# Optimization experiments

Measured on AMD Instinct MI355X. Metric: run time of the kernel, lower is better.

## Reference

```python
import jax, jax.numpy as jnp
import numpy as np

C = 300      # caption feature dim (word2vec)
OQK = 75     # in_dim // k = 300 // 4 -> query/key channels
H = 128      # adapt_img_hidden (base_proj dim)
LAT = 1024   # image latent size
EPS = 1e-5   # BatchNorm eps


def setup_inputs() -> dict:
    key = jax.random.key(0)
    ks = jax.random.split(key, 16)
    r = lambda i, shape, s=0.05: jax.random.normal(ks[i], shape, dtype=jnp.float32) * s
    return dict(
        img_embed=jax.random.normal(ks[0], (128, 36, LAT), dtype=jnp.float32),
        cap_embed=jax.random.normal(ks[1], (64, 32, C), dtype=jnp.float32),
        # adapt_img: Linear(1024, 128)
        adapt_W=r(2, (H, LAT)), adapt_b=jnp.zeros((H,), jnp.float32),
        # query ProjConv1d: kernel Linear(H, OQK*C), bias Linear(H, OQK), BatchNorm1d(OQK)
        qk_W=r(3, (OQK * C, H)), qk_b=r(4, (OQK * C,)),
        qb_W=r(5, (OQK, H)), qb_b=jnp.zeros((OQK,), jnp.float32),
        q_bn_s=jnp.ones((OQK,), jnp.float32), q_bn_b=jnp.zeros((OQK,), jnp.float32),
        # key ProjConv1d
        kk_W=r(6, (OQK * C, H)), kk_b=r(7, (OQK * C,)),
        kb_W=r(8, (OQK, H)), kb_b=jnp.zeros((OQK,), jnp.float32),
        k_bn_s=jnp.ones((OQK,), jnp.float32), k_bn_b=jnp.zeros((OQK,), jnp.float32),
        # value ProjConv1d: kernel Linear(H, C*C), bias Linear(H, C), BatchNorm1d(C)
        vk_W=r(9, (C * C, H)), vk_b=r(10, (C * C,)),
        vb_W=r(11, (C, H)), vb_b=jnp.zeros((C,), jnp.float32),
        v_bn_s=jnp.ones((C,), jnp.float32), v_bn_b=jnp.zeros((C,), jnp.float32),
        gamma=jnp.float32(0.5),  # residual attention gate (torch inits to 0; 0.5 exercises the path)
        # sim_proj MLP: 300 -> 512 -> 64 -> 1 with BatchNorm+ReLU (dropout = identity at eval)
        W1=r(12, (512, C)), b1=jnp.zeros((512,), jnp.float32),
        bn1_s=jnp.ones((512,), jnp.float32), bn1_b=jnp.zeros((512,), jnp.float32),
        W2=r(13, (64, 512)), b2=jnp.zeros((64,), jnp.float32),
        bn2_s=jnp.ones((64,), jnp.float32), bn2_b=jnp.zeros((64,), jnp.float32),
        W3=r(14, (1, 64)), b3=jnp.zeros((1,), jnp.float32),
    )


def _bn_kernel(kern, s, b):
    # torch: BatchNorm1d(out)(kernel.permute(1,0,2)) with kernel (out, in, ks=1)
    # -> per out-channel stats over the `in` axis (train-mode batch stats)
    mu = kern.mean(axis=1, keepdims=True)
    var = kern.var(axis=1, keepdims=True)
    return (kern - mu) / jnp.sqrt(var + EPS) * s[:, None] + b[:, None]


def _bn_batch(x, s, b):
    # BatchNorm1d over batch axis of (N, C) activations (train-mode stats)
    mu = x.mean(axis=0, keepdims=True)
    var = x.var(axis=0, keepdims=True)
    return (x - mu) / jnp.sqrt(var + EPS) * s + b


def reference(img_embed, cap_embed, adapt_W, adapt_b,
              qk_W, qk_b, qb_W, qb_b, q_bn_s, q_bn_b,
              kk_W, kk_b, kb_W, kb_b, k_bn_s, k_bn_b,
              vk_W, vk_b, vb_W, vb_b, v_bn_s, v_bn_b,
              gamma, W1, b1, bn1_s, bn1_b, W2, b2, bn2_s, bn2_b, W3, b3):
    cap = cap_embed.transpose(0, 2, 1)                      # (Bc, C, T)
    img_mean = img_embed.transpose(0, 2, 1).mean(-1)        # (Bi, LAT): mean over 36 regions
    base = img_mean @ adapt_W.T + adapt_b                   # (Bi, H)

    def per_image(bp):
        # hypernet-generated 1x1 conv kernels, batchnorm-normalized
        Kq = _bn_kernel((qk_W @ bp + qk_b).reshape(OQK, C), q_bn_s, q_bn_b)
        Kk = _bn_kernel((kk_W @ bp + kk_b).reshape(OQK, C), k_bn_s, k_bn_b)
        Kv = _bn_kernel((vk_W @ bp + vk_b).reshape(C, C), v_bn_s, v_bn_b)
        bq = qb_W @ bp + qb_b
        bk = kb_W @ bp + kb_b
        bv = vb_W @ bp + vb_b
        q = jnp.einsum('oc,nct->not', Kq, cap) + bq[:, None]    # (Bc, OQK, T)
        k = jnp.einsum('oc,nct->not', Kk, cap) + bk[:, None]    # (Bc, OQK, T)
        v = jnp.einsum('oc,nct->not', Kv, cap) + bv[:, None]    # (Bc, C, T)
        attn = jax.nn.softmax(jnp.einsum('not,nos->nts', q, k), axis=-1)  # (Bc, T, T)
        sa = jnp.einsum('ncs,nts->nct', v, attn)                # out = V @ attn^T
        x = (gamma * sa + cap).max(-1)                          # (Bc, C): max-pool over tokens
        h = jax.nn.relu(_bn_batch(x @ W1.T + b1, bn1_s, bn1_b))
        h = jax.nn.relu(_bn_batch(h @ W2.T + b2, bn2_s, bn2_b))
        return (h @ W3.T + b3)[:, 0]                            # (Bc,)

    return jax.vmap(per_image)(base)                            # (Bi, Bc)
```

## Files before the change

kernel.cpp:

```cpp
#include <hip/hip_runtime.h>
#include <math.h>

#define EPSB 1e-5f

static const long OFS_BASE  = 0;
static const long OFS_BALL  = 16384;
static const long OFS_CAPB  = 212992;
static const long OFS_RAWP  = 868352;
static const long OFS_X     = 15286272;
static const long OFS_H2    = 17743872;
static const long OFS_BASP  = 18268160;
static const long OFS_H1    = OFS_RAWP;

using bf16x8 = __attribute__((ext_vector_type(8))) __bf16;
using f32x4  = __attribute__((ext_vector_type(4))) float;
#define MFMA16(a, b, c) __builtin_amdgcn_mfma_f32_16x16x32_bf16(a, b, c, 0, 0, 0)

__device__ inline ushort f2bf(float f) {
  const unsigned u = __float_as_uint(f);
  return (ushort)((u + 0x7FFFu + ((u >> 16) & 1u)) >> 16);
}
__device__ inline float bf2f(ushort h) { return __uint_as_float(((unsigned)h) << 16); }

__global__ void __launch_bounds__(256) k_mb(const float* __restrict__ img,
                                            const float* __restrict__ W,
                                            const float* __restrict__ b,
                                            float* __restrict__ base) {
  __shared__ float m_s[1024];
  __shared__ float part[128];
  const int i = blockIdx.x, tid = threadIdx.x;
#pragma unroll
  for (int lc = 0; lc < 4; ++lc) {
    const int l = lc * 256 + tid;
    const float* p = img + (size_t)i * 36864 + l;
    float s = 0.f;
#pragma unroll
    for (int r = 0; r < 36; ++r) s += p[r * 1024];
    m_s[l] = s * (1.0f / 36.0f);
  }
  __syncthreads();
  const int o = tid & 127, hk = tid >> 7;
  const float* wr = W + (size_t)o * 1024 + hk * 512;
  const float* ms = m_s + hk * 512;
  float acc = 0.f;
#pragma unroll 4
  for (int l = 0; l < 512; ++l) acc = fmaf(ms[l], wr[l], acc);
  if (hk) part[o] = acc;
  __syncthreads();
  if (!hk) base[i * 128 + o] = acc + part[o] + b[o];
}

__global__ void __launch_bounds__(256) k_prep(
    const float* __restrict__ qbW, const float* __restrict__ qbb,
    const float* __restrict__ kbW, const float* __restrict__ kbb,
    const float* __restrict__ vbW, const float* __restrict__ vbb,
    const float* __restrict__ base, float* __restrict__ ball,
    const float* __restrict__ cap, ushort* __restrict__ capP,
    ushort* __restrict__ basP) {
  __shared__ float shm[32 * 301];
  const int bid = blockIdx.x, tid = threadIdx.x;
  if (bid < 256) {
    const int i = bid >> 1;
    if (tid < 128) shm[tid] = base[i * 128 + tid];
    __syncthreads();
    const int o = (bid & 1) * 256 + tid;
    const float* Wr = nullptr;
    float bb = 0.0f;
    if (o < 75)                   { Wr = qbW + (size_t)o * 128;         bb = qbb[o]; }
    else if (o >= 96 && o < 171)  { Wr = kbW + (size_t)(o - 96) * 128;  bb = kbb[o - 96]; }
    else if (o >= 192 && o < 492) { Wr = vbW + (size_t)(o - 192) * 128; bb = vbb[o - 192]; }
    float acc = 0.0f;
    if (Wr) {
#pragma unroll 4
      for (int h = 0; h < 128; ++h) acc = fmaf(Wr[h], shm[h], acc);
      acc += bb;
    }
    ball[i * 512 + o] = acc;
  } else if (bid < 320) {
    const int n = bid - 256;
    const float* capn = cap + (size_t)n * 9600;
    {
      const int r = tid >> 3, c8 = tid & 7;
      for (int m = 0; m < 38; ++m) {
        const int c = c8 + 8 * m;
        if (c < 300) shm[r * 301 + c] = capn[r * 300 + c];
      }
    }
    __syncthreads();
    ushort* dst = capP + (size_t)n * 20480;
    for (int u = 0; u < 10; ++u) {
      const int ul = tid + 256 * u;
      const int unit = ul >> 6, lane = ul & 63;
      const int nt = unit / 20, rem = unit % 20;
      const int ks = rem >> 1, pl = rem & 1;
      const int kg = lane >> 4, lr = lane & 15;
      const int t = nt * 16 + lr;
      ushort o8[8];
#pragma unroll
      for (int e = 0; e < 8; ++e) {
        const int c = 32 * ks + 8 * kg + e;
        const float val = (c < 300) ? shm[t * 301 + c] : 0.f;
        const ushort hi = f2bf(val);
        o8[e] = pl ? f2bf(val - bf2f(hi)) : hi;
      }
      uint4 pk;
      pk.x = (uint)o8[0] | ((uint)o8[1] << 16);
      pk.y = (uint)o8[2] | ((uint)o8[3] << 16);
      pk.z = (uint)o8[4] | ((uint)o8[5] << 16);
      pk.w = (uint)o8[6] | ((uint)o8[7] << 16);
      *reinterpret_cast<uint4*>(dst + unit * 512 + lane * 8) = pk;
    }
  } else {
    const int half = bid - 320;
    for (int m = 0; m < 8; ++m) {
      const int u = tid + 256 * m;
      const int ln = u & 63, unit = u >> 6;
      const int it = unit >> 3, ks = (unit >> 1) & 3, pl = unit & 1;
      const int i = half * 64 + it * 16 + (ln & 15);
      const int h = ks * 32 + (ln >> 4) * 8;
      ushort o8[8];
#pragma unroll
      for (int e = 0; e < 8; ++e) {
        const float v = base[(size_t)i * 128 + h + e];
        const ushort hi = f2bf(v);
        o8[e] = pl ? f2bf(v - bf2f(hi)) : hi;
      }
      uint4 pk;
      pk.x = (uint)o8[0] | ((uint)o8[1] << 16);
      pk.y = (uint)o8[2] | ((uint)o8[3] << 16);
      pk.z = (uint)o8[4] | ((uint)o8[5] << 16);
      pk.w = (uint)o8[6] | ((uint)o8[7] << 16);
      *reinterpret_cast<uint4*>(basP + (size_t)(half * 32 + unit) * 512 + ln * 8) = pk;
    }
  }
}

__global__ void __launch_bounds__(256) k_hyp4(
    const float* __restrict__ qkW, const float* __restrict__ qkb,
    const float* __restrict__ kkW, const float* __restrict__ kkb,
    const float* __restrict__ vkW, const float* __restrict__ vkb,
    const float* __restrict__ qs, const float* __restrict__ qb,
    const float* __restrict__ ks_, const float* __restrict__ kb_,
    const float* __restrict__ vs, const float* __restrict__ vb,
    const ushort* __restrict__ basP, ushort* __restrict__ kall) {
  __shared__ float smem[19760];
  __shared__ float scl[64], shf[64];
  const int g = blockIdx.x, half = blockIdx.y, tid = threadIdx.x;
  const int i0g = half * 64;
  const int ot = g >> 4, lr = g & 15;
  const bool isV = (g >= 192);
  if ((g >= 80 && g < 96) || (g >= 176 && g < 192)) return;

  const float* Wb = nullptr;
  const float* bvec = nullptr;
  float bns = 0.f, bnb = 0.f;
  if (g < 75)                    { Wb = qkW + (size_t)g * 38400;          bvec = qkb + g * 300;          bns = qs[g];        bnb = qb[g]; }
  else if (g >= 96 && g < 171)   { Wb = kkW + (size_t)(g - 96) * 38400;   bvec = kkb + (g - 96) * 300;   bns = ks_[g - 96];  bnb = kb_[g - 96]; }
  else if (g >= 192 && g < 492)  { Wb = vkW + (size_t)(g - 192) * 38400;  bvec = vkb + (g - 192) * 300;  bns = vs[g - 192];  bnb = vb[g - 192]; }

  if (!Wb) {
    const uint4 z = make_uint4(0, 0, 0, 0);
    if (!isV) {
      for (int m = 0; m < 20; ++m) {
        const int idx = tid + 256 * m;
        const int ii = idx & 63, zz = idx >> 6;
        const int kg2 = zz & 3, pl = (zz >> 2) & 1, ks2 = zz >> 3;
        const size_t off = (size_t)(i0g + ii) * 225280 +
                           (size_t)(ot * 20 + ks2 * 2 + pl) * 512 + (kg2 * 16 + lr) * 8;
        *reinterpret_cast<uint4*>(kall + off) = z;
      }
    } else {
      for (int m = 0; m < 10; ++m) {
        const int idx = tid + 256 * m;
        const int ii = idx & 63, zz = idx >> 6;
        const int kg2 = zz & 3, ks2 = zz >> 2;
        const size_t off = (size_t)(i0g + ii) * 225280 +
                           (size_t)(240 + (ot - 12) * 10 + ks2) * 512 + (kg2 * 16 + lr) * 8;
        *reinterpret_cast<uint4*>(kall + off) = z;
      }
    }
    return;
  }

  const int lane = tid & 63, w = tid >> 6;
  const int lrow = lane & 15, kg = lane >> 4;
  ushort* Af = reinterpret_cast<ushort*>(smem + 9760);

  f32x4 acc[19];
#pragma unroll
  for (int ct = 0; ct < 19; ++ct) acc[ct] = (f32x4){0.f, 0.f, 0.f, 0.f};

  for (int hc = 0; hc < 4; ++hc) {
    __syncthreads();
    for (int m = 0; m < 10; ++m) {
      const int u = tid + 256 * m;
      if (u < 2432) {
        const int c = u >> 3, h4 = (u & 7) * 4;
        float4 wv = make_float4(0.f, 0.f, 0.f, 0.f);
        if (c < 300) wv = *reinterpret_cast<const float4*>(Wb + (size_t)c * 128 + hc * 32 + h4);
        smem[(h4 + 0) * 305 + c] = wv.x;
        smem[(h4 + 1) * 305 + c] = wv.y;
        smem[(h4 + 2) * 305 + c] = wv.z;
        smem[(h4 + 3) * 305 + c] = wv.w;
      }
    }
    __syncthreads();
    for (int m = 0; m < 5; ++m) {
      const int u = tid + 256 * m;
      if (u < 1216) {
        const int ln = u & 63, ct = u >> 6;
        const int cc = ct * 16 + (ln & 15);
        const int hb = (ln >> 4) * 8;
        ushort h8[8], l8[8];
#pragma unroll
        for (int e = 0; e < 8; ++e) {
          const float v = smem[(hb + e) * 305 + cc];
          const ushort hi = f2bf(v);
          h8[e] = hi;
          l8[e] = f2bf(v - bf2f(hi));
        }
        uint4 ph, pl4;
        ph.x = (uint)h8[0] | ((uint)h8[1] << 16);
        ph.y = (uint)h8[2] | ((uint)h8[3] << 16);
        ph.z = (uint)h8[4] | ((uint)h8[5] << 16);
        ph.w = (uint)h8[6] | ((uint)h8[7] << 16);
        pl4.x = (uint)l8[0] | ((uint)l8[1] << 16);
        pl4.y = (uint)l8[2] | ((uint)l8[3] << 16);
        pl4.z = (uint)l8[4] | ((uint)l8[5] << 16);
        pl4.w = (uint)l8[6] | ((uint)l8[7] << 16);
        *reinterpret_cast<uint4*>(&Af[(ct * 2 + 0) * 512 + ln * 8]) = ph;
        *reinterpret_cast<uint4*>(&Af[(ct * 2 + 1) * 512 + ln * 8]) = pl4;
      }
    }
    const bf16x8 Bh = *reinterpret_cast<const bf16x8*>(
        basP + (size_t)(half * 32 + w * 8 + hc * 2 + 0) * 512 + lane * 8);
    const bf16x8 Bl = *reinterpret_cast<const bf16x8*>(
        basP + (size_t)(half * 32 + w * 8 + hc * 2 + 1) * 512 + lane * 8);
    __syncthreads();
#pragma unroll
    for (int ct = 0; ct < 19; ++ct) {
      const bf16x8 Ah = *reinterpret_cast<const bf16x8*>(&Af[(ct * 2 + 0) * 512 + lane * 8]);
      const bf16x8 Al = *reinterpret_cast<const bf16x8*>(&Af[(ct * 2 + 1) * 512 + lane * 8]);
      acc[ct] = MFMA16(Ah, Bh, acc[ct]);
      acc[ct] = MFMA16(Ah, Bl, acc[ct]);
      acc[ct] = MFMA16(Al, Bh, acc[ct]);
    }
  }
  __syncthreads();
#pragma unroll
  for (int ct = 0; ct < 19; ++ct)
#pragma unroll
    for (int r = 0; r < 4; ++r) {
      const int c = ct * 16 + kg * 4 + r;
      if (c < 300) smem[c * 65 + w * 16 + lrow] = acc[ct][r] + bvec[c];
    }
  __syncthreads();
  {
    const int si = tid >> 2, p = tid & 3;
    float s1 = 0.f, s2 = 0.f;
    for (int c = p; c < 300; c += 4) {
      const float x = smem[c * 65 + si];
      s1 += x;
      s2 += x * x;
    }
    s1 += __shfl_xor(s1, 1); s2 += __shfl_xor(s2, 1);
    s1 += __shfl_xor(s1, 2); s2 += __shfl_xor(s2, 2);
    const float mu = s1 * (1.0f / 300.0f);
    const float var = s2 * (1.0f / 300.0f) - mu * mu;
    const float scale = bns / sqrtf(var + EPSB);
    if (p == 0) { scl[si] = scale; shf[si] = bnb - mu * scale; }
  }
  __syncthreads();
  if (!isV) {
    for (int m = 0; m < 20; ++m) {
      const int idx = tid + 256 * m;
      const int ii = idx & 63, zz = idx >> 6;
      const int kg2 = zz & 3, pl = (zz >> 2) & 1, ks2 = zz >> 3;
      const float sc = scl[ii], sh = shf[ii];
      ushort o8[8];
#pragma unroll
      for (int e = 0; e < 8; ++e) {
        const int c = ks2 * 32 + kg2 * 8 + e;
        float val = 0.f;
        if (c < 300) val = fmaf(smem[c * 65 + ii], sc, sh);
        const ushort hi = f2bf(val);
        o8[e] = pl ? f2bf(val - bf2f(hi)) : hi;
      }
      uint4 pk;
      pk.x = (uint)o8[0] | ((uint)o8[1] << 16);
      pk.y = (uint)o8[2] | ((uint)o8[3] << 16);
      pk.z = (uint)o8[4] | ((uint)o8[5] << 16);
      pk.w = (uint)o8[6] | ((uint)o8[7] << 16);
      const size_t off = (size_t)(i0g + ii) * 225280 +
                         (size_t)(ot * 20 + ks2 * 2 + pl) * 512 + (kg2 * 16 + lr) * 8;
      *reinterpret_cast<uint4*>(kall + off) = pk;
    }
  } else {
    for (int m = 0; m < 10; ++m) {
      const int idx = tid + 256 * m;
      const int ii = idx & 63, zz = idx >> 6;
      const int kg2 = zz & 3, ks2 = zz >> 2;
      const float sc = scl[ii], sh = shf[ii];
      ushort o8[8];
#pragma unroll
      for (int e = 0; e < 8; ++e) {
        const int c = ks2 * 32 + kg2 * 8 + e;
        float val = 0.f;
        if (c < 300) val = fmaf(smem[c * 65 + ii], sc, sh);
        o8[e] = f2bf(val);
      }
      uint4 pk;
      pk.x = (uint)o8[0] | ((uint)o8[1] << 16);
      pk.y = (uint)o8[2] | ((uint)o8[3] << 16);
      pk.z = (uint)o8[4] | ((uint)o8[5] << 16);
      pk.w = (uint)o8[6] | ((uint)o8[7] << 16);
      const size_t off = (size_t)(i0g + ii) * 225280 +
                         (size_t)(240 + (ot - 12) * 10 + ks2) * 512 + (kg2 * 16 + lr) * 8;
      *reinterpret_cast<uint4*>(kall + off) = pk;
    }
  }
}

__global__ void __launch_bounds__(256, 4) k_attn12(
    const float* __restrict__ cap, const ushort* __restrict__ kall,
    const ushort* __restrict__ capP, const float* __restrict__ ball,
    const float* __restrict__ gptr, float* __restrict__ x_all) {
  __shared__ ushort qkp[24 * 512];
  __shared__ float sc_s[32 * 36];
  __shared__ ushort at_p[2 * 2 * 64 * 8];
  const int bid = blockIdx.x;
  const int xcd = bid & 7, q = bid >> 3;
  const int i = xcd * 16 + (q >> 6), n = q & 63;
  const int tid = threadIdx.x;
  const int lane = tid & 63, w = tid >> 6;
  const int lrow = lane & 15, kg = lane >> 4;
  const float gamma = gptr[0];
  const ushort* kpL = kall + (size_t)i * 225280 + lane * 8;
  const ushort* cpL = capP + (size_t)n * 20480 + lane * 8;
  const float* bal = ball + i * 512;
  const bool oddw = (w & 1);

  {
    f32x4 acc[3][2];
#pragma unroll
    for (int a = 0; a < 3; ++a)
#pragma unroll
      for (int b2 = 0; b2 < 2; ++b2) acc[a][b2] = (f32x4){0.f, 0.f, 0.f, 0.f};
    bf16x8 AhA[3], AlA[3], AhB[3], AlB[3];
#pragma unroll
    for (int mt = 0; mt < 3; ++mt)
      if (!oddw || mt < 2) {
        const ushort* p = kpL + (size_t)((w * 3 + mt) * 20) * 512;
        AhA[mt] = *reinterpret_cast<const bf16x8*>(p);
        AlA[mt] = *reinterpret_cast<const bf16x8*>(p + 512);
      }
#pragma unroll
    for (int kp = 0; kp < 5; ++kp) {
      {
        const int ks = 2 * kp;
        bf16x8 Bh[2], Bl[2];
#pragma unroll
        for (int nt = 0; nt < 2; ++nt) {
          const ushort* p = cpL + (size_t)(nt * 20 + ks * 2) * 512;
          Bh[nt] = *reinterpret_cast<const bf16x8*>(p);
          Bl[nt] = *reinterpret_cast<const bf16x8*>(p + 512);
        }
#pragma unroll
        for (int mt = 0; mt < 3; ++mt)
          if (!oddw || mt < 2) {
            const ushort* p = kpL + (size_t)((w * 3 + mt) * 20 + (ks + 1) * 2) * 512;
            AhB[mt] = *reinterpret_cast<const bf16x8*>(p);
            AlB[mt] = *reinterpret_cast<const bf16x8*>(p + 512);
          }
#pragma unroll
        for (int mt = 0; mt < 3; ++mt)
          if (!oddw || mt < 2)
#pragma unroll
            for (int nt = 0; nt < 2; ++nt) {
              acc[mt][nt] = MFMA16(AhA[mt], Bh[nt], acc[mt][nt]);
              acc[mt][nt] = MFMA16(AhA[mt], Bl[nt], acc[mt][nt]);
              acc[mt][nt] = MFMA16(AlA[mt], Bh[nt], acc[mt][nt]);
            }
      }
      {
        const int ks = 2 * kp + 1;
        bf16x8 Bh[2], Bl[2];
#pragma unroll
        for (int nt = 0; nt < 2; ++nt) {
          const ushort* p = cpL + (size_t)(nt * 20 + ks * 2) * 512;
          Bh[nt] = *reinterpret_cast<const bf16x8*>(p);
          Bl[nt] = *reinterpret_cast<const bf16x8*>(p + 512);
        }
        if (kp < 4) {
#pragma unroll
          for (int mt = 0; mt < 3; ++mt)
            if (!oddw || mt < 2) {
              const ushort* p = kpL + (size_t)((w * 3 + mt) * 20 + (ks + 1) * 2) * 512;
              AhA[mt] = *reinterpret_cast<const bf16x8*>(p);
              AlA[mt] = *reinterpret_cast<const bf16x8*>(p + 512);
            }
        }
#pragma unroll
        for (int mt = 0; mt < 3; ++mt)
          if (!oddw || mt < 2)
#pragma unroll
            for (int nt = 0; nt < 2; ++nt) {
              acc[mt][nt] = MFMA16(AhB[mt], Bh[nt], acc[mt][nt]);
              acc[mt][nt] = MFMA16(AhB[mt], Bl[nt], acc[mt][nt]);
              acc[mt][nt] = MFMA16(AlB[mt], Bh[nt], acc[mt][nt]);
            }
      }
    }
#pragma unroll
    for (int mt = 0; mt < 3; ++mt)
#pragma unroll
      for (int nt = 0; nt < 2; ++nt) {
        const int og0 = w * 48 + mt * 16 + kg * 4;
        const int os0 = (w < 2) ? og0 : og0 - 96;
        const int ub = ((w < 2) ? 0 : 12) + nt * 6 + (os0 >> 5) * 2;
        const int lp = ((os0 & 31) >> 3) * 16 + lrow;
        const int e0 = os0 & 7;
        ushort h4[4], l4[4];
#pragma unroll
        for (int r = 0; r < 4; ++r) {
          const float val = acc[mt][nt][r] + bal[og0 + r];
          const ushort hi = f2bf(val);
          h4[r] = hi;
          l4[r] = f2bf(val - bf2f(hi));
        }
        uint2 ph, pl2;
        ph.x = (uint)h4[0] | ((uint)h4[1] << 16);
        ph.y = (uint)h4[2] | ((uint)h4[3] << 16);
        pl2.x = (uint)l4[0] | ((uint)l4[1] << 16);
        pl2.y = (uint)l4[2] | ((uint)l4[3] << 16);
        *reinterpret_cast<uint2*>(&qkp[(ub + 0) * 512 + lp * 8 + e0]) = ph;
        *reinterpret_cast<uint2*>(&qkp[(ub + 1) * 512 + lp * 8 + e0]) = pl2;
      }
  }
  __syncthreads();

  {
    const int tt = w >> 1, st = w & 1;
    bf16x8 Aq[3][2], Bk[3][2];
#pragma unroll
    for (int k3 = 0; k3 < 3; ++k3)
#pragma unroll
      for (int pl = 0; pl < 2; ++pl) {
        Aq[k3][pl] = *reinterpret_cast<const bf16x8*>(&qkp[(tt * 6 + k3 * 2 + pl) * 512 + lane * 8]);
        Bk[k3][pl] = *reinterpret_cast<const bf16x8*>(&qkp[(12 + st * 6 + k3 * 2 + pl) * 512 + lane * 8]);
      }
    f32x4 D = (f32x4){0.f, 0.f, 0.f, 0.f};
#pragma unroll
    for (int k3 = 0; k3 < 3; ++k3) {
      D = MFMA16(Aq[k3][0], Bk[k3][0], D);
      D = MFMA16(Aq[k3][0], Bk[k3][1], D);
      D = MFMA16(Aq[k3][1], Bk[k3][0], D);
      D = MFMA16(Aq[k3][1], Bk[k3][1], D);
    }
#pragma unroll
    for (int r = 0; r < 4; ++r)
      sc_s[(tt * 16 + kg * 4 + r) * 36 + st * 16 + lrow] = D[r];
  }
  __syncthreads();

  {
    const int sg = tid & 7, tq = tid >> 3;
    const int s0 = sg * 4;
    const float4 sv = *reinterpret_cast<const float4*>(&sc_s[tq * 36 + s0]);
    float sc[4] = {sv.x, sv.y, sv.z, sv.w};
    float m = fmaxf(fmaxf(sc[0], sc[1]), fmaxf(sc[2], sc[3]));
    m = fmaxf(m, __shfl_xor(m, 1));
    m = fmaxf(m, __shfl_xor(m, 2));
    m = fmaxf(m, __shfl_xor(m, 4));
    float ev[4], ssum = 0.f;
#pragma unroll
    for (int u = 0; u < 4; ++u) { ev[u] = expf(sc[u] - m); ssum += ev[u]; }
    ssum += __shfl_xor(ssum, 1);
    ssum += __shfl_xor(ssum, 2);
    ssum += __shfl_xor(ssum, 4);
    const float inv = 1.0f / ssum;
    const int tt = tq >> 4, lrp = tq & 15, kgp = sg >> 1, eb = (sg & 1) * 4;
    ushort h4[4], l4[4];
#pragma unroll
    for (int u = 0; u < 4; ++u) {
      const float val = ev[u] * inv;
      const ushort hi = f2bf(val);
      h4[u] = hi;
      l4[u] = f2bf(val - bf2f(hi));
    }
    uint2 ph, pl2;
    ph.x = (uint)h4[0] | ((uint)h4[1] << 16);
    ph.y = (uint)h4[2] | ((uint)h4[3] << 16);
    pl2.x = (uint)l4[0] | ((uint)l4[1] << 16);
    pl2.y = (uint)l4[2] | ((uint)l4[3] << 16);
    *reinterpret_cast<uint2*>(&at_p[((tt * 2 + 0) * 64 + kgp * 16 + lrp) * 8 + eb]) = ph;
    *reinterpret_cast<uint2*>(&at_p[((tt * 2 + 1) * 64 + kgp * 16 + lrp) * 8 + eb]) = pl2;
  }
  __syncthreads();

  ushort* vt = qkp;
#pragma unroll
  for (int ch = 0; ch < 2; ++ch) {
    const int TB = 12 + ch * 12;
    const int RB = TB * 16;
    const int nmt = ch ? 2 : 3;
    f32x4 vacc[3][2];
#pragma unroll
    for (int a = 0; a < 3; ++a)
#pragma unroll
      for (int b2 = 0; b2 < 2; ++b2) vacc[a][b2] = (f32x4){0.f, 0.f, 0.f, 0.f};
    bf16x8 AvA[3], AvB[3];
    for (int mi = 0; mi < nmt; ++mi)
      AvA[mi] = *reinterpret_cast<const bf16x8*>(
          kpL + (size_t)(240 + (TB - 12 + w + mi * 4) * 10) * 512);
#pragma unroll
    for (int kp = 0; kp < 5; ++kp) {
      {
        const int ks = 2 * kp;
        bf16x8 Ch[2];
#pragma unroll
        for (int nt = 0; nt < 2; ++nt)
          Ch[nt] = *reinterpret_cast<const bf16x8*>(cpL + (size_t)(nt * 20 + ks * 2) * 512);
        for (int mi = 0; mi < nmt; ++mi)
          AvB[mi] = *reinterpret_cast<const bf16x8*>(
              kpL + (size_t)(240 + (TB - 12 + w + mi * 4) * 10 + ks + 1) * 512);
        for (int mi = 0; mi < nmt; ++mi)
#pragma unroll
          for (int nt = 0; nt < 2; ++nt)
            vacc[mi][nt] = MFMA16(Ch[nt], AvA[mi], vacc[mi][nt]);
      }
      {
        const int ks = 2 * kp + 1;
        bf16x8 Ch[2];
#pragma unroll
        for (int nt = 0; nt < 2; ++nt)
          Ch[nt] = *reinterpret_cast<const bf16x8*>(cpL + (size_t)(nt * 20 + ks * 2) * 512);
        if (kp < 4) {
          for (int mi = 0; mi < nmt; ++mi)
            AvA[mi] = *reinterpret_cast<const bf16x8*>(
                kpL + (size_t)(240 + (TB - 12 + w + mi * 4) * 10 + ks + 1) * 512);
        }
        for (int mi = 0; mi < nmt; ++mi)
#pragma unroll
          for (int nt = 0; nt < 2; ++nt)
            vacc[mi][nt] = MFMA16(Ch[nt], AvB[mi], vacc[mi][nt]);
      }
    }
    if (ch) __syncthreads();
    for (int mi = 0; mi < nmt; ++mi) {
      const int tile = w + mi * 4;
      const float bb = bal[RB + tile * 16 + lrow];
#pragma unroll
      for (int nt = 0; nt < 2; ++nt) {
        const int lpv = (nt * 2 + (kg >> 1)) * 16 + lrow;
        const int e0v = (kg & 1) * 4;
        ushort h4[4], l4[4];
#pragma unroll
        for (int r = 0; r < 4; ++r) {
          const float val = vacc[mi][nt][r] + bb;
          const ushort hi = f2bf(val);
          h4[r] = hi;
          l4[r] = f2bf(val - bf2f(hi));
        }
        uint2 ph, pl2;
        ph.x = (uint)h4[0] | ((uint)h4[1] << 16);
        ph.y = (uint)h4[2] | ((uint)h4[3] << 16);
        pl2.x = (uint)l4[0] | ((uint)l4[1] << 16);
        pl2.y = (uint)l4[2] | ((uint)l4[3] << 16);
        *reinterpret_cast<uint2*>(&vt[((tile * 2 + 0) * 64 + lpv) * 8 + e0v]) = ph;
        *reinterpret_cast<uint2*>(&vt[((tile * 2 + 1) * 64 + lpv) * 8 + e0v]) = pl2;
      }
    }
    __syncthreads();
    {
      bf16x8 ah[2], al[2];
#pragma unroll
      for (int tt = 0; tt < 2; ++tt) {
        ah[tt] = *reinterpret_cast<const bf16x8*>(&at_p[((tt * 2 + 0) * 64 + lane) * 8]);
        al[tt] = *reinterpret_cast<const bf16x8*>(&at_p[((tt * 2 + 1) * 64 + lane) * 8]);
      }
      const int npw = ch ? 2 : 3;
      for (int j = 0; j < npw; ++j) {
        const int ct = w * npw + j;
        const int c0 = ch * 192 + ct * 16 + (lane >> 4) * 4;
        const bf16x8 vh  = *reinterpret_cast<const bf16x8*>(&vt[((ct * 2 + 0) * 64 + lane) * 8]);
        const bf16x8 vl8 = *reinterpret_cast<const bf16x8*>(&vt[((ct * 2 + 1) * 64 + lane) * 8]);
        f32x4 a0 = (f32x4){0.f, 0.f, 0.f, 0.f}, a1 = (f32x4){0.f, 0.f, 0.f, 0.f};
        a0 = MFMA16(vh, ah[0], a0);
        a0 = MFMA16(vh, al[0], a0);
        a0 = MFMA16(vl8, ah[0], a0);
        a1 = MFMA16(vh, ah[1], a1);
        a1 = MFMA16(vh, al[1], a1);
        a1 = MFMA16(vl8, ah[1], a1);
        if (c0 < 300) {
          const int t0 = lane & 15;
          const float4 c4a = *reinterpret_cast<const float4*>(&cap[(size_t)n * 9600 + t0 * 300 + c0]);
          const float4 c4b = *reinterpret_cast<const float4*>(&cap[(size_t)n * 9600 + (t0 + 16) * 300 + c0]);
          float mx[4];
          mx[0] = fmaxf(fmaf(gamma, a0[0], c4a.x), fmaf(gamma, a1[0], c4b.x));
          mx[1] = fmaxf(fmaf(gamma, a0[1], c4a.y), fmaf(gamma, a1[1], c4b.y));
          mx[2] = fmaxf(fmaf(gamma, a0[2], c4a.z), fmaf(gamma, a1[2], c4b.z));
          mx[3] = fmaxf(fmaf(gamma, a0[3], c4a.w), fmaf(gamma, a1[3], c4b.w));
#pragma unroll
          for (int mmask = 1; mmask < 16; mmask <<= 1)
#pragma unroll
            for (int r = 0; r < 4; ++r) mx[r] = fmaxf(mx[r], __shfl_xor(mx[r], mmask));
          if ((lane & 15) == 0)
            *reinterpret_cast<float4*>(&x_all[((size_t)i * 64 + n) * 300 + c0]) =
                make_float4(mx[0], mx[1], mx[2], mx[3]);
        }
      }
    }
  }
}

__global__ void __launch_bounds__(256, 4) k_h1b(
    const float* __restrict__ x_all, const float* __restrict__ W1,
    const float* __restrict__ b1, const float* __restrict__ bn1s,
    const float* __restrict__ bn1b, float* __restrict__ h1) {
  __shared__ float xt[32 * 68];
  __shared__ float wt[32 * 132];
  __shared__ float sc1[128], sh1[128];
  const int ec = blockIdx.x, i = blockIdx.y, tid = threadIdx.x;
  const int e0c = ec * 128;
  const int eg = tid & 15, ng = tid >> 4;
  const int e0 = eg * 8, n0 = ng * 4;
  float acc[4][8] = {};
  for (int cb = 0; cb < 10; ++cb) {
    const int c0 = cb * 32;
    __syncthreads();
    for (int k = 0; k < 8; ++k) {
      const int idx = tid + 256 * k;
      const int nn = idx >> 5, cl = idx & 31;
      const int c = c0 + cl;
      xt[cl * 68 + nn] = (c < 300) ? x_all[((size_t)i * 64 + nn) * 300 + c] : 0.0f;
    }
    for (int k = 0; k < 16; ++k) {
      const int idx = tid + 256 * k;
      const int ee = idx >> 5, cl = idx & 31;
      const int c = c0 + cl;
      wt[cl * 132 + ee] = (c < 300) ? W1[(size_t)(e0c + ee) * 300 + c] : 0.0f;
    }
    __syncthreads();
#pragma unroll 4
    for (int cl = 0; cl < 32; ++cl) {
      const float4 xv = *reinterpret_cast<const float4*>(&xt[cl * 68 + n0]);
      const float4 wa = *reinterpret_cast<const float4*>(&wt[cl * 132 + e0]);
      const float4 wb = *reinterpret_cast<const float4*>(&wt[cl * 132 + e0 + 4]);
      const float xv4[4] = {xv.x, xv.y, xv.z, xv.w};
      const float wv8[8] = {wa.x, wa.y, wa.z, wa.w, wb.x, wb.y, wb.z, wb.w};
#pragma unroll
      for (int u = 0; u < 4; ++u)
#pragma unroll
        for (int v = 0; v < 8; ++v) acc[u][v] = fmaf(xv4[u], wv8[v], acc[u][v]);
    }
  }
  float b1v[8];
#pragma unroll
  for (int v = 0; v < 8; ++v) b1v[v] = b1[e0c + e0 + v];
  float val[4][8];
#pragma unroll
  for (int u = 0; u < 4; ++u)
#pragma unroll
    for (int v = 0; v < 8; ++v) val[u][v] = acc[u][v] + b1v[v];
  __syncthreads();
  float* ps1 = xt;
  float* ps2 = wt;
#pragma unroll
  for (int v = 0; v < 8; ++v) {
    float su = 0.f, sq = 0.f;
#pragma unroll
    for (int u = 0; u < 4; ++u) { su += val[u][v]; sq += val[u][v] * val[u][v]; }
    ps1[ng * 132 + e0 + v] = su;
    ps2[ng * 132 + e0 + v] = sq;
  }
  __syncthreads();
  if (tid < 128) {
    const int e = tid;
    float s1 = 0.f, s2 = 0.f;
#pragma unroll 4
    for (int gq = 0; gq < 16; ++gq) { s1 += ps1[gq * 132 + e]; s2 += ps2[gq * 132 + e]; }
    const float mu = s1 * (1.0f / 64.0f);
    const float var = s2 * (1.0f / 64.0f) - mu * mu;
    const float scale = bn1s[e0c + e] / sqrtf(var + EPSB);
    sc1[e] = scale;
    sh1[e] = bn1b[e0c + e] - mu * scale;
  }
  __syncthreads();
#pragma unroll
  for (int u = 0; u < 4; ++u) {
    float o8[8];
#pragma unroll
    for (int v = 0; v < 8; ++v)
      o8[v] = fmaxf(fmaf(val[u][v], sc1[e0 + v], sh1[e0 + v]), 0.0f);
    float* dst = h1 + ((size_t)i * 64 + n0 + u) * 512 + e0c + e0;
    *reinterpret_cast<float4*>(dst) = make_float4(o8[0], o8[1], o8[2], o8[3]);
    *reinterpret_cast<float4*>(dst + 4) = make_float4(o8[4], o8[5], o8[6], o8[7]);
  }
}

__global__ void __launch_bounds__(256) k_h2(
    const float* __restrict__ h1, const float* __restrict__ W2,
    const float* __restrict__ b2, float* __restrict__ h2buf) {
  __shared__ float h1s[32 * 517];
  const int jn = blockIdx.x, i = blockIdx.y, tid = threadIdx.x;
  const int bn = jn * 32;
  for (int m = 0; m < 64; ++m) {
    const int idx = tid + 256 * m;
    h1s[(idx >> 9) * 517 + (idx & 511)] = h1[((size_t)i * 64 + bn) * 512 + idx];
  }
  __syncthreads();
  const int dg = tid & 15, ng2 = tid >> 4;
  const int d0 = dg * 4, n0 = ng2 * 2;
  float a0[4] = {}, a1[4] = {};
#pragma unroll 4
  for (int e = 0; e < 512; ++e) {
    const float h0 = h1s[n0 * 517 + e];
    const float h1v = h1s[(n0 + 1) * 517 + e];
#pragma unroll
    for (int v = 0; v < 4; ++v) {
      const float wv = W2[(size_t)(d0 + v) * 512 + e];
      a0[v] = fmaf(h0, wv, a0[v]);
      a1[v] = fmaf(h1v, wv, a1[v]);
    }
  }
  const float4 bb = *reinterpret_cast<const float4*>(&b2[d0]);
  float* dst0 = h2buf + ((size_t)i * 64 + bn + n0) * 64 + d0;
  *reinterpret_cast<float4*>(dst0) = make_float4(a0[0] + bb.x, a0[1] + bb.y, a0[2] + bb.z, a0[3] + bb.w);
  *reinterpret_cast<float4*>(dst0 + 64) = make_float4(a1[0] + bb.x, a1[1] + bb.y, a1[2] + bb.z, a1[3] + bb.w);
}

__global__ void __launch_bounds__(256) k_out(
    const float* __restrict__ h2buf, const float* __restrict__ bn2s,
    const float* __restrict__ bn2b, const float* __restrict__ W3,
    const float* __restrict__ b3, float* __restrict__ out) {
  __shared__ float h2s[64 * 65];
  const int i = blockIdx.x, tid = threadIdx.x;
  for (int m = 0; m < 16; ++m) {
    const int idx = tid + 256 * m;
    h2s[(idx >> 6) * 65 + (idx & 63)] = h2buf[(size_t)i * 4096 + idx];
  }
  __syncthreads();
  if (tid < 64) {
    const int d = tid;
    float s1 = 0.f, s2 = 0.f;
    for (int nn = 0; nn < 64; ++nn) {
      const float v = h2s[nn * 65 + d];
      s1 += v;
      s2 += v * v;
    }
    const float mu = s1 * (1.0f / 64.0f);
    const float var = s2 * (1.0f / 64.0f) - mu * mu;
    const float scale = bn2s[d] / sqrtf(var + EPSB);
    const float shift = bn2b[d] - mu * scale;
    for (int nn = 0; nn < 64; ++nn)
      h2s[nn * 65 + d] = fmaxf(fmaf(h2s[nn * 65 + d], scale, shift), 0.0f);
  }
  __syncthreads();
  if (tid < 64) {
    const int nn = tid;
    float acc = b3[0];
    for (int d = 0; d < 64; ++d) acc = fmaf(h2s[nn * 65 + d], W3[d], acc);
    out[i * 64 + nn] = acc;
  }
}

extern "C" void kernel_launch(void* const* d_in, const int* in_sizes, int n_in,
                              void* d_out, int out_size, void* d_ws, size_t ws_size,
                              hipStream_t stream) {
  const float* img  = (const float*)d_in[0];
  const float* cap  = (const float*)d_in[1];
  const float* adW  = (const float*)d_in[2];
  const float* adb  = (const float*)d_in[3];
  const float* qkW  = (const float*)d_in[4];
  const float* qkb  = (const float*)d_in[5];
  const float* qbW  = (const float*)d_in[6];
  const float* qbb  = (const float*)d_in[7];
  const float* qbns = (const float*)d_in[8];
  const float* qbnb = (const float*)d_in[9];
  const float* kkW  = (const float*)d_in[10];
  const float* kkb  = (const float*)d_in[11];
  const float* kbW  = (const float*)d_in[12];
  const float* kbb  = (const float*)d_in[13];
  const float* kbns = (const float*)d_in[14];
  const float* kbnb = (const float*)d_in[15];
  const float* vkW  = (const float*)d_in[16];
  const float* vkb  = (const float*)d_in[17];
  const float* vbW  = (const float*)d_in[18];
  const float* vbb  = (const float*)d_in[19];
  const float* vbns = (const float*)d_in[20];
  const float* vbnb = (const float*)d_in[21];
  const float* gamma= (const float*)d_in[22];
  const float* W1   = (const float*)d_in[23];
  const float* b1   = (const float*)d_in[24];
  const float* bn1s = (const float*)d_in[25];
  const float* bn1b = (const float*)d_in[26];
  const float* W2   = (const float*)d_in[27];
  const float* b2   = (const float*)d_in[28];
  const float* bn2s = (const float*)d_in[29];
  const float* bn2b = (const float*)d_in[30];
  const float* W3   = (const float*)d_in[31];
  const float* b3   = (const float*)d_in[32];

  float* ws    = (float*)d_ws;
  float* base  = ws + OFS_BASE;
  float* ball  = ws + OFS_BALL;
  ushort* capP = (ushort*)(ws + OFS_CAPB);
  ushort* kall = (ushort*)(ws + OFS_RAWP);
  float* x_all = ws + OFS_X;
  float* h2buf = ws + OFS_H2;
  ushort* basP = (ushort*)(ws + OFS_BASP);
  float* h1    = ws + OFS_H1;
  float* out   = (float*)d_out;

  k_mb<<<128, 256, 0, stream>>>(img, adW, adb, base);
  k_prep<<<322, 256, 0, stream>>>(qbW, qbb, kbW, kbb, vbW, vbb, base, ball, cap, capP, basP);
  k_hyp4<<<dim3(512, 2), 256, 0, stream>>>(qkW, qkb, kkW, kkb, vkW, vkb,
                                           qbns, qbnb, kbns, kbnb, vbns, vbnb, basP, kall);
  k_attn12<<<8192, 256, 0, stream>>>(cap, kall, capP, ball, gamma, x_all);
  k_h1b<<<dim3(4, 128), 256, 0, stream>>>(x_all, W1, b1, bn1s, bn1b, h1);
  k_h2<<<dim3(2, 128), 256, 0, stream>>>(h1, W2, b2, h2buf);
  k_out<<<128, 256, 0, stream>>>(h2buf, bn2s, bn2b, W3, b3, out);
}
```

Before: 486.0 us.

## Load hypernet weights straight into MFMA fragments, removing LDS staging and barriers

```diff
diff --git a/kernel.cpp b/kernel.cpp
--- a/kernel.cpp
+++ b/kernel.cpp
@@ -17,8 +17,8 @@
 #define MFMA16(a, b, c) __builtin_amdgcn_mfma_f32_16x16x32_bf16(a, b, c, 0, 0, 0)
 
 __device__ inline ushort f2bf(float f) {
-  const unsigned u = __float_as_uint(f);
-  return (ushort)((u + 0x7FFFu + ((u >> 16) & 1u)) >> 16);
+  const __bf16 h = (__bf16)f;
+  return __builtin_bit_cast(ushort, h);
 }
 __device__ inline float bf2f(ushort h) { return __uint_as_float(((unsigned)h) << 16); }
 
@@ -135,7 +135,7 @@
   }
 }
 
-__global__ void __launch_bounds__(256) k_hyp4(
+__global__ void __launch_bounds__(256) k_hyp5(
     const float* __restrict__ qkW, const float* __restrict__ qkb,
     const float* __restrict__ kkW, const float* __restrict__ kkb,
     const float* __restrict__ vkW, const float* __restrict__ vkb,
@@ -143,7 +143,7 @@
     const float* __restrict__ ks_, const float* __restrict__ kb_,
     const float* __restrict__ vs, const float* __restrict__ vb,
     const ushort* __restrict__ basP, ushort* __restrict__ kall) {
-  __shared__ float smem[19760];
+  __shared__ float smem[19500];
   __shared__ float scl[64], shf[64];
   const int g = blockIdx.x, half = blockIdx.y, tid = threadIdx.x;
   const int i0g = half * 64;
@@ -184,76 +184,71 @@
 
   const int lane = tid & 63, w = tid >> 6;
   const int lrow = lane & 15, kg = lane >> 4;
-  ushort* Af = reinterpret_cast<ushort*>(smem + 9760);
-
-  f32x4 acc[19];
-#pragma unroll
-  for (int ct = 0; ct < 19; ++ct) acc[ct] = (f32x4){0.f, 0.f, 0.f, 0.f};
-
+  const int CT0 = w * 5;
+
+  f32x4 acc[5][4];
+#pragma unroll
+  for (int t = 0; t < 5; ++t)
+#pragma unroll
+    for (int it = 0; it < 4; ++it) acc[t][it] = (f32x4){0.f, 0.f, 0.f, 0.f};
+
+#pragma unroll
   for (int hc = 0; hc < 4; ++hc) {
-    __syncthreads();
-    for (int m = 0; m < 10; ++m) {
-      const int u = tid + 256 * m;
-      if (u < 2432) {
-        const int c = u >> 3, h4 = (u & 7) * 4;
-        float4 wv = make_float4(0.f, 0.f, 0.f, 0.f);
-        if (c < 300) wv = *reinterpret_cast<const float4*>(Wb + (size_t)c * 128 + hc * 32 + h4);
-        smem[(h4 + 0) * 305 + c] = wv.x;
-        smem[(h4 + 1) * 305 + c] = wv.y;
-        smem[(h4 + 2) * 305 + c] = wv.z;
-        smem[(h4 + 3) * 305 + c] = wv.w;
-      }
-    }
-    __syncthreads();
-    for (int m = 0; m < 5; ++m) {
-      const int u = tid + 256 * m;
-      if (u < 1216) {
-        const int ln = u & 63, ct = u >> 6;
-        const int cc = ct * 16 + (ln & 15);
-        const int hb = (ln >> 4) * 8;
-        ushort h8[8], l8[8];
+    bf16x8 Bh[4], Bl[4];
+#pragma unroll
+    for (int it = 0; it < 4; ++it) {
+      Bh[it] = *reinterpret_cast<const bf16x8*>(
+          basP + (size_t)(half * 32 + it * 8 + hc * 2 + 0) * 512 + lane * 8);
+      Bl[it] = *reinterpret_cast<const bf16x8*>(
+          basP + (size_t)(half * 32 + it * 8 + hc * 2 + 1) * 512 + lane * 8);
+    }
+#pragma unroll
+    for (int t = 0; t < 5; ++t) {
+      const int ct = CT0 + t;
+      if (ct < 19) {
+        const int c = ct * 16 + lrow;
+        float wv[8];
+        if (c < 300) {
+          const float4 w0 = *reinterpret_cast<const float4*>(Wb + (size_t)c * 128 + hc * 32 + kg * 8);
+          const float4 w1 = *reinterpret_cast<const float4*>(Wb + (size_t)c * 128 + hc * 32 + kg * 8 + 4);
+          wv[0] = w0.x; wv[1] = w0.y; wv[2] = w0.z; wv[3] = w0.w;
+          wv[4] = w1.x; wv[5] = w1.y; wv[6] = w1.z; wv[7] = w1.w;
+        } else {
+#pragma unroll
+          for (int e = 0; e < 8; ++e) wv[e] = 0.f;
+        }
+        bf16x8 Ah, Al;
 #pragma unroll
         for (int e = 0; e < 8; ++e) {
-          const float v = smem[(hb + e) * 305 + cc];
-          const ushort hi = f2bf(v);
-          h8[e] = hi;
-          l8[e] = f2bf(v - bf2f(hi));
-        }
-        uint4 ph, pl4;
-        ph.x = (uint)h8[0] | ((uint)h8[1] << 16);
-        ph.y = (uint)h8[2] | ((uint)h8[3] << 16);
-        ph.z = (uint)h8[4] | ((uint)h8[5] << 16);
-        ph.w = (uint)h8[6] | ((uint)h8[7] << 16);
-        pl4.x = (uint)l8[0] | ((uint)l8[1] << 16);
-        pl4.y = (uint)l8[2] | ((uint)l8[3] << 16);
-        pl4.z = (uint)l8[4] | ((uint)l8[5] << 16);
-        pl4.w = (uint)l8[6] | ((uint)l8[7] << 16);
-        *reinterpret_cast<uint4*>(&Af[(ct * 2 + 0) * 512 + ln * 8]) = ph;
-        *reinterpret_cast<uint4*>(&Af[(ct * 2 + 1) * 512 + ln * 8]) = pl4;
-      }
-    }
-    const bf16x8 Bh = *reinterpret_cast<const bf16x8*>(
-        basP + (size_t)(half * 32 + w * 8 + hc * 2 + 0) * 512 + lane * 8);
-    const bf16x8 Bl = *reinterpret_cast<const bf16x8*>(
-        basP + (size_t)(half * 32 + w * 8 + hc * 2 + 1) * 512 + lane * 8);
-    __syncthreads();
-#pragma unroll
-    for (int ct = 0; ct < 19; ++ct) {
-      const bf16x8 Ah = *reinterpret_cast<const bf16x8*>(&Af[(ct * 2 + 0) * 512 + lane * 8]);
-      const bf16x8 Al = *reinterpret_cast<const bf16x8*>(&Af[(ct * 2 + 1) * 512 + lane * 8]);
-      acc[ct] = MFMA16(Ah, Bh, acc[ct]);
-      acc[ct] = MFMA16(Ah, Bl, acc[ct]);
-      acc[ct] = MFMA16(Al, Bh, acc[ct]);
-    }
-  }
-  __syncthreads();
-#pragma unroll
-  for (int ct = 0; ct < 19; ++ct)
-#pragma unroll
-    for (int r = 0; r < 4; ++r) {
-      const int c = ct * 16 + kg * 4 + r;
-      if (c < 300) smem[c * 65 + w * 16 + lrow] = acc[ct][r] + bvec[c];
-    }
+          const __bf16 h = (__bf16)wv[e];
+          Ah[e] = h;
+          Al[e] = (__bf16)(wv[e] - (float)h);
+        }
+#pragma unroll
+        for (int it = 0; it < 4; ++it) {
+          acc[t][it] = MFMA16(Ah, Bh[it], acc[t][it]);
+          acc[t][it] = MFMA16(Ah, Bl[it], acc[t][it]);
+          acc[t][it] = MFMA16(Al, Bh[it], acc[t][it]);
+        }
+      }
+    }
+  }
+#pragma unroll
+  for (int t = 0; t < 5; ++t) {
+    const int ct = CT0 + t;
+    if (ct < 19) {
+#pragma unroll
+      for (int r = 0; r < 4; ++r) {
+        const int c = ct * 16 + kg * 4 + r;
+        if (c < 300) {
+          const float bv = bvec[c];
+#pragma unroll
+          for (int it = 0; it < 4; ++it)
+            smem[c * 65 + it * 16 + lrow] = acc[t][it][r] + bv;
+        }
+      }
+    }
+  }
   __syncthreads();
   {
     const int si = tid >> 2, p = tid & 3;
@@ -815,7 +810,7 @@
 
   k_mb<<<128, 256, 0, stream>>>(img, adW, adb, base);
   k_prep<<<322, 256, 0, stream>>>(qbW, qbb, kbW, kbb, vbW, vbb, base, ball, cap, capP, basP);
-  k_hyp4<<<dim3(512, 2), 256, 0, stream>>>(qkW, qkb, kkW, kkb, vkW, vkb,
+  k_hyp5<<<dim3(512, 2), 256, 0, stream>>>(qkW, qkb, kkW, kkb, vkW, vkb,
                                            qbns, qbnb, kbns, kbnb, vbns, vbnb, basP, kall);
   k_attn12<<<8192, 256, 0, stream>>>(cap, kall, capP, ball, gamma, x_all);
   k_h1b<<<dim3(4, 128), 256, 0, stream>>>(x_all, W1, b1, bn1s, bn1b, h1);
```

Result: faster. 469.7 us (-3.3%).
